# Performance work log

Measured on AMD Instinct MI355X. Metric: run time of the kernel, lower is better.

## Reference

```python
import jax, jax.numpy as jnp
import numpy as np

NEG_INF = -9e15  # matches torch's -9000000000000000.0 mask value
ALPHA = 0.2      # LeakyReLU negative slope


def setup_inputs() -> dict:
    key = jax.random.key(0)
    k1, k2, k3, k4 = jax.random.split(key, 4)
    B, N, Fin, Fout, H = 32, 512, 256, 64, 8
    x = jax.random.normal(k1, (B, N, Fin), dtype=jnp.float32)
    adj = (jax.random.uniform(k2, (B, N, N)) < 0.5).astype(jnp.float32)
    # W: Linear(in_features, out_features*n_heads, bias=False) weight, stored as (Fin, Fout*H)
    W = jax.random.normal(k3, (Fin, Fout * H), dtype=jnp.float32) / np.sqrt(Fin).astype(np.float32)
    # a: attention vector per head over concat(src,dst) features -> (H, 2*Fout)
    a = jax.random.normal(k4, (H, 2 * Fout), dtype=jnp.float32) * 0.1
    return {"x": x, "adj": adj, "W": W, "a": a}


def reference(x, adj, W, a):
    # x: (B,N,Fin), adj: (B,N,N), W: (Fin, H*F), a: (H, 2F)
    B, N, _ = x.shape
    H, twoF = a.shape
    F = twoF // 2
    h = (x @ W).reshape(B, N, H, F)  # (B,N,H,F)
    # Decompose concat-score: e_ij = lrelu(h_i . a_src + h_j . a_dst) -- same math
    # as (cat(h_i,h_j) * a).sum(-1) without materializing (B,N,N,H,2F).
    s_src = jnp.einsum('bnhf,hf->bnh', h, a[:, :F])  # (B,N,H)
    s_dst = jnp.einsum('bnhf,hf->bnh', h, a[:, F:])  # (B,N,H)
    e = s_src[:, :, None, :] + s_dst[:, None, :, :]  # (B,N,N,H)
    e = jax.nn.leaky_relu(e, negative_slope=ALPHA)
    e = jnp.where(adj[..., None] > 0, e, NEG_INF)
    attn = jax.nn.softmax(e, axis=2)  # softmax over neighbors j (dim=2)
    # dropout omitted (eval mode / p effectively 0 for the reference baseline)
    h_prime = jnp.einsum('bijh,bjhf->bihf', attn, h)  # (B,N,H,F)
    return h_prime.reshape(B, N, H * F)  # concat=True
```

## Files before the change

### kernel.cpp

```cpp
#include <hip/hip_runtime.h>
#include <hip/hip_bf16.h>


#define ALPHA  0.2f
#define ESCALE 1.4426950408889634f

typedef __bf16 bf16x8 __attribute__((ext_vector_type(8)));
typedef __bf16 bf16x4 __attribute__((ext_vector_type(4)));
typedef float  f32x4  __attribute__((ext_vector_type(4)));

#if __has_builtin(__builtin_amdgcn_exp2f)
#define EXP2(x) __builtin_amdgcn_exp2f(x)
#else
#define EXP2(x) exp2f(x)
#endif

#define HT_STRIDE 520
#define WT_STRIDE 264

struct Smem {
    __bf16 hT[64][HT_STRIDE];
    __bf16 WT[64][WT_STRIDE];
    float  ssrc[512], sdst[512];
    float  asrc[64], adst[64];
};

__device__ inline bf16x8 ld8(const float* p) {
    float4 a0 = *(const float4*)p;
    float4 a1 = *(const float4*)(p + 4);
    bf16x8 r;
    r[0]=(__bf16)a0.x; r[1]=(__bf16)a0.y; r[2]=(__bf16)a0.z; r[3]=(__bf16)a0.w;
    r[4]=(__bf16)a1.x; r[5]=(__bf16)a1.y; r[6]=(__bf16)a1.z; r[7]=(__bf16)a1.w;
    return r;
}

__global__ __launch_bounds__(512, 1) void k_gat(const float* __restrict__ x,
                                                const float* __restrict__ adj,
                                                const float* __restrict__ W,
                                                const float* __restrict__ a,
                                                float* __restrict__ out) {
    __shared__ Smem sm;
    const int b = blockIdx.x, h = blockIdx.y;
    const int tid  = threadIdx.x;
    const int wave = tid >> 6, lane = tid & 63;
    const int quad = lane >> 4, col = lane & 15;

    if (tid < 128) {
        float v = a[h * 128 + tid] * ESCALE;
        if (tid < 64) sm.asrc[tid] = v; else sm.adst[tid - 64] = v;
    }
    {
        int c = tid & 63, k0 = tid >> 6;
        #pragma unroll 4
        for (int t = 0; t < 32; ++t)
            sm.WT[c][k0 + t * 8] = (__bf16)W[(long)(k0 + t * 8) * 512 + h * 64 + c];
    }
    __syncthreads();

    {
        const float* xb = x + (long)b * 512 * 256;
        f32x4 acc[4][4] = {};
        for (int ks = 0; ks < 8; ++ks) {
            int k0 = ks * 32 + quad * 8;
            bf16x8 av[4], bv[4];
            #pragma unroll
            for (int it = 0; it < 4; ++it)
                av[it] = ld8(xb + (long)(wave * 64 + it * 16 + col) * 256 + k0);
            #pragma unroll
            for (int nt = 0; nt < 4; ++nt)
                bv[nt] = *(const bf16x8*)(&sm.WT[nt * 16 + col][k0]);
            #pragma unroll
            for (int it = 0; it < 4; ++it)
                #pragma unroll
                for (int nt = 0; nt < 4; ++nt)
                    acc[it][nt] = __builtin_amdgcn_mfma_f32_16x16x32_bf16(av[it], bv[nt], acc[it][nt], 0, 0, 0);
        }
        #pragma unroll
        for (int it = 0; it < 4; ++it)
            #pragma unroll
            for (int nt = 0; nt < 4; ++nt) {
                int f = nt * 16 + col;
                int j = wave * 64 + it * 16 + quad * 4;
                bf16x4 pk = { (__bf16)acc[it][nt][0], (__bf16)acc[it][nt][1],
                              (__bf16)acc[it][nt][2], (__bf16)acc[it][nt][3] };
                *(bf16x4*)(&sm.hT[f][j]) = pk;
            }
    }
    __syncthreads();

    {
        float as = 0.f, ad = 0.f;
        #pragma unroll 8
        for (int f = 0; f < 64; ++f) {
            float v = (float)sm.hT[f][tid];
            as += v * sm.asrc[f];
            ad += v * sm.adst[f];
        }
        sm.ssrc[tid] = as;
        sm.sdst[tid] = ad;
    }
    __syncthreads();

    {
        float si[4];
        const float* arow[4];
        #pragma unroll
        for (int it = 0; it < 4; ++it) {
            int i = wave * 64 + it * 16 + col;
            si[it]   = sm.ssrc[i];
            arow[it] = adj + ((long)b * 512 + i) * 512;
        }
        bf16x8 ones;
        #pragma unroll
        for (int u = 0; u < 8; ++u) ones[u] = (__bf16)1.0f;

        f32x4 acc[4][4] = {};
        f32x4 accs[4]   = {};
        float4 pa0[4], pa1[4];
        #pragma unroll
        for (int it = 0; it < 4; ++it) {
            pa0[it] = *(const float4*)(arow[it] + quad * 8);
            pa1[it] = *(const float4*)(arow[it] + quad * 8 + 4);
        }
        for (int ks = 0; ks < 16; ++ks) {
            int j0 = ks * 32 + quad * 8;
            f32x4 s0 = *(const f32x4*)&sm.sdst[j0];
            f32x4 s1 = *(const f32x4*)&sm.sdst[j0 + 4];
            float sd[8] = {s0[0],s0[1],s0[2],s0[3],s1[0],s1[1],s1[2],s1[3]};
            float am[4][8];
            #pragma unroll
            for (int it = 0; it < 4; ++it) {
                am[it][0]=pa0[it].x; am[it][1]=pa0[it].y;
                am[it][2]=pa0[it].z; am[it][3]=pa0[it].w;
                am[it][4]=pa1[it].x; am[it][5]=pa1[it].y;
                am[it][6]=pa1[it].z; am[it][7]=pa1[it].w;
            }
            if (ks < 15) {
                #pragma unroll
                for (int it = 0; it < 4; ++it) {
                    pa0[it] = *(const float4*)(arow[it] + j0 + 32);
                    pa1[it] = *(const float4*)(arow[it] + j0 + 36);
                }
            }
            bf16x8 P[4];
            #pragma unroll
            for (int it = 0; it < 4; ++it)
                #pragma unroll
                for (int u = 0; u < 8; ++u) {
                    float e = si[it] + sd[u];
                    float l = fmaxf(e, ALPHA * e);
                    float p = am[it][u] * EXP2(l);
                    P[it][u] = (__bf16)p;
                }
            bf16x8 bv[4];
            #pragma unroll
            for (int nt = 0; nt < 4; ++nt)
                bv[nt] = *(const bf16x8*)(&sm.hT[nt * 16 + col][j0]);
            #pragma unroll
            for (int it = 0; it < 4; ++it) {
                #pragma unroll
                for (int nt = 0; nt < 4; ++nt)
                    acc[it][nt] = __builtin_amdgcn_mfma_f32_16x16x32_bf16(P[it], bv[nt], acc[it][nt], 0, 0, 0);
                accs[it] = __builtin_amdgcn_mfma_f32_16x16x32_bf16(P[it], ones, accs[it], 0, 0, 0);
            }
        }
        #pragma unroll
        for (int it = 0; it < 4; ++it)
            #pragma unroll
            for (int r = 0; r < 4; ++r) {
                float s = accs[it][r];
                float inv = (s > 0.f) ? 1.0f / s : 0.f;
                int i = wave * 64 + it * 16 + quad * 4 + r;
                float* orow = out + ((long)b * 512 + i) * 512 + h * 64;
                #pragma unroll
                for (int nt = 0; nt < 4; ++nt)
                    orow[nt * 16 + col] = acc[it][nt][r] * inv;
            }
    }
}

extern "C" void kernel_launch(void* const* d_in, const int* in_sizes, int n_in,
                              void* d_out, int out_size, void* d_ws, size_t ws_size,
                              hipStream_t stream) {
    const float* x   = (const float*)d_in[0];
    const float* adj = (const float*)d_in[1];
    const float* W   = (const float*)d_in[2];
    const float* a   = (const float*)d_in[3];
    float* out = (float*)d_out;
    (void)d_ws; (void)ws_size;

    k_gat<<<dim3(32, 8), 512, 0, stream>>>(x, adj, W, a, out);
}
```

Before: 140.9 us.

## Factor exp of attention scores into per-node products, swizzle hT, deepen adj prefetch

```diff
diff --git a/kernel.cpp b/kernel.cpp
--- a/kernel.cpp
+++ b/kernel.cpp
@@ -15,13 +15,12 @@
 #define EXP2(x) exp2f(x)
 #endif
 
-#define HT_STRIDE 520
 #define WT_STRIDE 264
 
 struct Smem {
-    __bf16 hT[64][HT_STRIDE];
+    __bf16 hT[64 * 512];
     __bf16 WT[64][WT_STRIDE];
-    float  ssrc[512], sdst[512];
+    float  E[512], G[512], F[512], H[512];
     float  asrc[64], adst[64];
 };
 
@@ -81,33 +80,38 @@
             for (int nt = 0; nt < 4; ++nt) {
                 int f = nt * 16 + col;
                 int j = wave * 64 + it * 16 + quad * 4;
+                int bb = j >> 3;
                 bf16x4 pk = { (__bf16)acc[it][nt][0], (__bf16)acc[it][nt][1],
                               (__bf16)acc[it][nt][2], (__bf16)acc[it][nt][3] };
-                *(bf16x4*)(&sm.hT[f][j]) = pk;
+                *(bf16x4*)(&sm.hT[f * 512 + ((bb ^ (f & 7)) << 3) + (j & 7)]) = pk;
             }
     }
     __syncthreads();
 
     {
         float as = 0.f, ad = 0.f;
+        int bb = tid >> 3, off = tid & 7;
         #pragma unroll 8
         for (int f = 0; f < 64; ++f) {
-            float v = (float)sm.hT[f][tid];
+            float v = (float)sm.hT[f * 512 + ((bb ^ (f & 7)) << 3) + off];
             as += v * sm.asrc[f];
             ad += v * sm.adst[f];
         }
-        sm.ssrc[tid] = as;
-        sm.sdst[tid] = ad;
+        sm.E[tid] = EXP2(as);
+        sm.G[tid] = EXP2(ALPHA * as);
+        sm.F[tid] = EXP2(ad);
+        sm.H[tid] = EXP2(ALPHA * ad);
     }
     __syncthreads();
 
     {
-        float si[4];
+        float EI[4], GI[4];
         const float* arow[4];
         #pragma unroll
         for (int it = 0; it < 4; ++it) {
             int i = wave * 64 + it * 16 + col;
-            si[it]   = sm.ssrc[i];
+            EI[it]   = sm.E[i];
+            GI[it]   = sm.G[i];
             arow[it] = adj + ((long)b * 512 + i) * 512;
         }
         bf16x8 ones;
@@ -116,46 +120,54 @@
 
         f32x4 acc[4][4] = {};
         f32x4 accs[4]   = {};
-        float4 pa0[4], pa1[4];
-        #pragma unroll
-        for (int it = 0; it < 4; ++it) {
-            pa0[it] = *(const float4*)(arow[it] + quad * 8);
-            pa1[it] = *(const float4*)(arow[it] + quad * 8 + 4);
-        }
+        float4 pa[2][4][2];
+        #pragma unroll
+        for (int d = 0; d < 2; ++d)
+            #pragma unroll
+            for (int it = 0; it < 4; ++it) {
+                pa[d][it][0] = *(const float4*)(arow[it] + d * 32 + quad * 8);
+                pa[d][it][1] = *(const float4*)(arow[it] + d * 32 + quad * 8 + 4);
+            }
         for (int ks = 0; ks < 16; ++ks) {
             int j0 = ks * 32 + quad * 8;
-            f32x4 s0 = *(const f32x4*)&sm.sdst[j0];
-            f32x4 s1 = *(const f32x4*)&sm.sdst[j0 + 4];
-            float sd[8] = {s0[0],s0[1],s0[2],s0[3],s1[0],s1[1],s1[2],s1[3]};
+            int cur = ks & 1;
             float am[4][8];
             #pragma unroll
             for (int it = 0; it < 4; ++it) {
-                am[it][0]=pa0[it].x; am[it][1]=pa0[it].y;
-                am[it][2]=pa0[it].z; am[it][3]=pa0[it].w;
-                am[it][4]=pa1[it].x; am[it][5]=pa1[it].y;
-                am[it][6]=pa1[it].z; am[it][7]=pa1[it].w;
-            }
-            if (ks < 15) {
+                am[it][0]=pa[cur][it][0].x; am[it][1]=pa[cur][it][0].y;
+                am[it][2]=pa[cur][it][0].z; am[it][3]=pa[cur][it][0].w;
+                am[it][4]=pa[cur][it][1].x; am[it][5]=pa[cur][it][1].y;
+                am[it][6]=pa[cur][it][1].z; am[it][7]=pa[cur][it][1].w;
+            }
+            if (ks < 14) {
                 #pragma unroll
                 for (int it = 0; it < 4; ++it) {
-                    pa0[it] = *(const float4*)(arow[it] + j0 + 32);
-                    pa1[it] = *(const float4*)(arow[it] + j0 + 36);
+                    pa[cur][it][0] = *(const float4*)(arow[it] + j0 + 64);
+                    pa[cur][it][1] = *(const float4*)(arow[it] + j0 + 68);
                 }
             }
+            f32x4 F0 = *(const f32x4*)&sm.F[j0];
+            f32x4 F1 = *(const f32x4*)&sm.F[j0 + 4];
+            f32x4 H0 = *(const f32x4*)&sm.H[j0];
+            f32x4 H1 = *(const f32x4*)&sm.H[j0 + 4];
+            float Fv[8] = {F0[0],F0[1],F0[2],F0[3],F1[0],F1[1],F1[2],F1[3]};
+            float Hv[8] = {H0[0],H0[1],H0[2],H0[3],H1[0],H1[1],H1[2],H1[3]};
             bf16x8 P[4];
             #pragma unroll
             for (int it = 0; it < 4; ++it)
                 #pragma unroll
                 for (int u = 0; u < 8; ++u) {
-                    float e = si[it] + sd[u];
-                    float l = fmaxf(e, ALPHA * e);
-                    float p = am[it][u] * EXP2(l);
+                    float ef = EI[it] * Fv[u];
+                    float gh = GI[it] * Hv[u];
+                    float p  = (ef > 1.0f ? ef : gh) * am[it][u];
                     P[it][u] = (__bf16)p;
                 }
             bf16x8 bv[4];
             #pragma unroll
-            for (int nt = 0; nt < 4; ++nt)
-                bv[nt] = *(const bf16x8*)(&sm.hT[nt * 16 + col][j0]);
+            for (int nt = 0; nt < 4; ++nt) {
+                int f = nt * 16 + col;
+                bv[nt] = *(const bf16x8*)(&sm.hT[f * 512 + (((ks * 4 + quad) ^ (f & 7)) << 3)]);
+            }
             #pragma unroll
             for (int it = 0; it < 4; ++it) {
                 #pragma unroll
```

After: 215.1 us. 52.7% more time.

## Pack adjacency into bitmask and factor exp of leaky-relu into products

Applied to the files above, without the earlier changes.

```diff
diff --git a/kernel.cpp b/kernel.cpp
--- a/kernel.cpp
+++ b/kernel.cpp
@@ -21,7 +21,7 @@
 struct Smem {
     __bf16 hT[64][HT_STRIDE];
     __bf16 WT[64][WT_STRIDE];
-    float  ssrc[512], sdst[512];
+    float  E[512], G[512], F[512], H[512];
     float  asrc[64], adst[64];
 };
 
@@ -34,8 +34,22 @@
     return r;
 }
 
+__global__ __launch_bounds__(512) void k_pack(const float* __restrict__ adj,
+                                              unsigned int* __restrict__ mask) {
+    const int i = blockIdx.x, b = blockIdx.y;
+    const int tid = threadIdx.x, wave = tid >> 6, lane = tid & 63;
+    float v = adj[((long)b * 512 + i) * 512 + tid];
+    unsigned long long m = __ballot(v > 0.f);
+    if (lane == 0) {
+        mask[(b * 16 + 2 * wave) * 512 + i]     = (unsigned int)m;
+        mask[(b * 16 + 2 * wave + 1) * 512 + i] = (unsigned int)(m >> 32);
+    }
+}
+
+template <bool USEM>
 __global__ __launch_bounds__(512, 1) void k_gat(const float* __restrict__ x,
                                                 const float* __restrict__ adj,
+                                                const unsigned int* __restrict__ mask,
                                                 const float* __restrict__ W,
                                                 const float* __restrict__ a,
                                                 float* __restrict__ out) {
@@ -96,60 +110,84 @@
             as += v * sm.asrc[f];
             ad += v * sm.adst[f];
         }
-        sm.ssrc[tid] = as;
-        sm.sdst[tid] = ad;
+        sm.E[tid] = EXP2(as);
+        sm.G[tid] = EXP2(ALPHA * as);
+        sm.F[tid] = EXP2(ad);
+        sm.H[tid] = EXP2(ALPHA * ad);
     }
     __syncthreads();
 
     {
-        float si[4];
+        const int qs = quad * 8;
+        float EI[4], GI[4];
+        int iw[4];
         const float* arow[4];
         #pragma unroll
         for (int it = 0; it < 4; ++it) {
             int i = wave * 64 + it * 16 + col;
-            si[it]   = sm.ssrc[i];
-            arow[it] = adj + ((long)b * 512 + i) * 512;
-        }
+            iw[it] = i;
+            EI[it] = sm.E[i];
+            GI[it] = sm.G[i];
+            if (!USEM) arow[it] = adj + ((long)b * 512 + i) * 512;
+        }
+        const unsigned int* mbase = mask + (long)b * 16 * 512;
         bf16x8 ones;
         #pragma unroll
         for (int u = 0; u < 8; ++u) ones[u] = (__bf16)1.0f;
 
         f32x4 acc[4][4] = {};
         f32x4 accs[4]   = {};
+        unsigned int pm[4];
         float4 pa0[4], pa1[4];
         #pragma unroll
         for (int it = 0; it < 4; ++it) {
-            pa0[it] = *(const float4*)(arow[it] + quad * 8);
-            pa1[it] = *(const float4*)(arow[it] + quad * 8 + 4);
+            if (USEM) pm[it] = mbase[iw[it]];
+            else {
+                pa0[it] = *(const float4*)(arow[it] + qs);
+                pa1[it] = *(const float4*)(arow[it] + qs + 4);
+            }
         }
         for (int ks = 0; ks < 16; ++ks) {
-            int j0 = ks * 32 + quad * 8;
-            f32x4 s0 = *(const f32x4*)&sm.sdst[j0];
-            f32x4 s1 = *(const f32x4*)&sm.sdst[j0 + 4];
-            float sd[8] = {s0[0],s0[1],s0[2],s0[3],s1[0],s1[1],s1[2],s1[3]};
+            int j0 = ks * 32 + qs;
+            unsigned int cm[4];
             float am[4][8];
             #pragma unroll
             for (int it = 0; it < 4; ++it) {
-                am[it][0]=pa0[it].x; am[it][1]=pa0[it].y;
-                am[it][2]=pa0[it].z; am[it][3]=pa0[it].w;
-                am[it][4]=pa1[it].x; am[it][5]=pa1[it].y;
-                am[it][6]=pa1[it].z; am[it][7]=pa1[it].w;
+                if (USEM) cm[it] = pm[it];
+                else {
+                    am[it][0]=pa0[it].x; am[it][1]=pa0[it].y;
+                    am[it][2]=pa0[it].z; am[it][3]=pa0[it].w;
+                    am[it][4]=pa1[it].x; am[it][5]=pa1[it].y;
+                    am[it][6]=pa1[it].z; am[it][7]=pa1[it].w;
+                }
             }
             if (ks < 15) {
                 #pragma unroll
                 for (int it = 0; it < 4; ++it) {
-                    pa0[it] = *(const float4*)(arow[it] + j0 + 32);
-                    pa1[it] = *(const float4*)(arow[it] + j0 + 36);
+                    if (USEM) pm[it] = mbase[(ks + 1) * 512 + iw[it]];
+                    else {
+                        pa0[it] = *(const float4*)(arow[it] + j0 + 32);
+                        pa1[it] = *(const float4*)(arow[it] + j0 + 36);
+                    }
                 }
             }
+            f32x4 F0 = *(const f32x4*)&sm.F[j0];
+            f32x4 F1 = *(const f32x4*)&sm.F[j0 + 4];
+            f32x4 H0 = *(const f32x4*)&sm.H[j0];
+            f32x4 H1 = *(const f32x4*)&sm.H[j0 + 4];
+            float Fv[8] = {F0[0],F0[1],F0[2],F0[3],F1[0],F1[1],F1[2],F1[3]};
+            float Hv[8] = {H0[0],H0[1],H0[2],H0[3],H1[0],H1[1],H1[2],H1[3]};
             bf16x8 P[4];
             #pragma unroll
             for (int it = 0; it < 4; ++it)
                 #pragma unroll
                 for (int u = 0; u < 8; ++u) {
-                    float e = si[it] + sd[u];
-                    float l = fmaxf(e, ALPHA * e);
-                    float p = am[it][u] * EXP2(l);
+                    float ef = EI[it] * Fv[u];
+                    float gh = GI[it] * Hv[u];
+                    float sel = ef > 1.0f ? ef : gh;
+                    float p;
+                    if (USEM) p = ((cm[it] >> (qs + u)) & 1u) ? sel : 0.0f;
+                    else      p = sel * am[it][u];
                     P[it][u] = (__bf16)p;
                 }
             bf16x8 bv[4];
@@ -187,7 +225,13 @@
     const float* W   = (const float*)d_in[2];
     const float* a   = (const float*)d_in[3];
     float* out = (float*)d_out;
-    (void)d_ws; (void)ws_size;
-
-    k_gat<<<dim3(32, 8), 512, 0, stream>>>(x, adj, W, a, out);
-}
+
+    const size_t MASK_BYTES = 32u * 16u * 512u * 4u;
+    if (ws_size >= MASK_BYTES) {
+        unsigned int* mask = (unsigned int*)d_ws;
+        k_pack<<<dim3(512, 32), 512, 0, stream>>>(adj, mask);
+        k_gat<true><<<dim3(32, 8), 512, 0, stream>>>(x, adj, mask, W, a, out);
+    } else {
+        k_gat<false><<<dim3(32, 8), 512, 0, stream>>>(x, adj, nullptr, W, a, out);
+    }
+}
```

New measurement: 144.0 us. 2.2% more time.
